# Kernel optimization log

Hardware: AMD Instinct MI355X
Metric: run time of the kernel (lower is better)

The kernel has to match this reference:

```python
import jax, jax.numpy as jnp
import numpy as np

N_NODES = 100_000
N_EDGES = 1_000_000
H = 128
NUM_STATES = 4
UPPER_T, LOWER_T, NUM_ITERS, TEMP_EVAL = 1.0, 0.1, 10000, 0.1


def temp_by_step(step, upper, lower, num_iters, temp_eval):
    # Python-level schedule: eval temp at step == -1, else linear anneal.
    if step == -1:
        return temp_eval
    frac = min(step / num_iters, 1.0)
    return upper + (lower - upper) * frac


def from_binary_states(states):
    # [*, k] bits -> integer id in [0, 2**k)
    weights = 2 ** jnp.arange(states.shape[-1])
    return (states * weights).sum(-1)


def setup_inputs() -> dict:
    key = jax.random.key(0)
    ks = jax.random.split(key, 20)
    N, E, h = N_NODES, N_EDGES, H
    node_states = jax.random.randint(ks[0], (N, NUM_STATES), 0, 2)
    edge_states = jax.random.randint(ks[1], (E, NUM_STATES), 0, 2)
    scalars = jax.random.normal(ks[2], (E, 1), jnp.float32)
    # first N edges are self-loops ordered by node id (required by the module's
    # node_scalars = scalars[src == dst] indexing convention)
    loops = jnp.arange(N)
    src = jax.random.randint(ks[3], (E - N,), 0, N)
    dst = jax.random.randint(ks[4], (E - N,), 0, N)
    dst = jnp.where(dst == src, (dst + 1) % N, dst)  # no accidental self-loops
    edge_index = jnp.stack([jnp.concatenate([loops, src]),
                            jnp.concatenate([loops, dst])])
    batched_reverse_idx = jax.random.randint(ks[5], (E,), 0, E)
    batch_scalars = jax.random.normal(ks[6], (E, 1, 1), jnp.float32)
    s = 0.02
    params = dict(
        node_emb=s * jax.random.normal(ks[7], (2 ** NUM_STATES, h), jnp.float32),
        edge_emb=s * jax.random.normal(ks[8], (2 ** NUM_STATES, h), jnp.float32),
        combine_W=s * jax.random.normal(ks[9], (2 * h, h), jnp.float32),
        combine_b=jnp.zeros((h,), jnp.float32),
        keep_W=s * jax.random.normal(ks[10], (h, 2), jnp.float32),
        keep_b=jnp.zeros((2,), jnp.float32),
        push_W=s * jax.random.normal(ks[11], (h, 2), jnp.float32),
        push_b=jnp.zeros((2,), jnp.float32),
        push_node_W=s * jax.random.normal(ks[12], (h, 2), jnp.float32),
        push_node_b=jnp.zeros((2,), jnp.float32),
        increment_W=s * jax.random.normal(ks[13], (h, 2), jnp.float32),
        increment_b=jnp.zeros((2,), jnp.float32),
    )
    return dict(node_states=node_states, edge_states=edge_states, scalars=scalars,
                edge_index=edge_index, batched_reverse_idx=batched_reverse_idx,
                batch_scalars=batch_scalars, processor_step=0, training_step=0,
                **params)


def reference(node_states, edge_states, scalars, edge_index, batched_reverse_idx,
              batch_scalars, processor_step, training_step,
              node_emb, edge_emb, combine_W, combine_b, keep_W, keep_b,
              push_W, push_b, push_node_W, push_node_b,
              increment_W, increment_b):
    N = node_states.shape[0]
    tau = temp_by_step(int(training_step), UPPER_T, LOWER_T, NUM_ITERS, TEMP_EVAL)
    # use_noise = config.use_noise (False) and training_step != -1 -> False

    node_fts = node_emb[from_binary_states(node_states)]   # [N, h]
    edge_fts = edge_emb[from_binary_states(edge_states)]   # [E, h]
    src, dst = edge_index[0], edge_index[1]
    fts = jnp.concatenate([edge_fts[batched_reverse_idx], node_fts[src]], axis=1)
    fts = fts @ combine_W + combine_b                       # [E, h]

    s = scalars.reshape(-1)                                 # [E]

    def pair_gumbel_first(W, b):
        # grouped (per-edge pair) softmax; take first component (== [::2])
        logits = (fts @ W + b) / tau                        # [E, 2]
        return jax.nn.softmax(logits, axis=-1)[:, 0]

    increment = 1.0 * pair_gumbel_first(increment_W, increment_b)
    keep = s * pair_gumbel_first(keep_W, keep_b)

    # push: first N edges are self-loops, self-loop of node i is edge i
    push_wo = pair_gumbel_first(push_W, push_b)
    push_w = pair_gumbel_first(push_node_W, push_node_b)
    node_scalars = s[:N]                                    # scalars at self-loops
    s_wo = s - node_scalars[dst]
    s_w = s_wo + node_scalars[src]
    acc = (jax.ops.segment_sum(push_wo * s_wo, dst, num_segments=N)
           + jax.ops.segment_sum(push_w * s_w, dst, num_segments=N))  # [N]
    edge_push = jnp.zeros_like(s).at[:N].set(acc)           # nonzero only on self-loops

    new_scalars = (increment + keep + edge_push)[:, None]   # [E, 1]
    target = batch_scalars[:, processor_step]               # [E, 1]
    loss = jnp.mean((target - new_scalars) ** 2)
    return new_scalars, loss
```

## Files before the change

kernel.cpp:

```cpp
#include <hip/hip_runtime.h>
#include <math.h>
#include <stdint.h>

#define N_NODES 100000
#define N_EDGES 1000000
#define HDIM 128
#define N_NONLOOP (N_EDGES - N_NODES)

typedef float  vfloat4 __attribute__((ext_vector_type(4)));
typedef int    vint4   __attribute__((ext_vector_type(4)));

__device__ __forceinline__ float get_invtau(const int* __restrict__ training_step) {
    int step = training_step[0];
    float tau;
    if (step == -1) {
        tau = 0.1f;
    } else {
        float frac = fminf((float)step / 10000.0f, 1.0f);
        tau = 1.0f + (0.1f - 1.0f) * frac;
    }
    return 1.0f / tau;
}

__device__ __forceinline__ float wave_reduce(float v) {
    #pragma unroll
    for (int off = 32; off > 0; off >>= 1) v += __shfl_down(v, off, 64);
    return v;
}

#define TAB_BLOCKS  33
#define NODE_BLOCKS 391
#define EI_BLOCKS   977

__global__ __launch_bounds__(256) void fused_pre(
    const int* __restrict__ node_states,
    const float* __restrict__ s,
    const int* __restrict__ edge_states,
    const float* __restrict__ node_emb,
    const float* __restrict__ edge_emb,
    const float* __restrict__ cW, const float* __restrict__ cb,
    const float* __restrict__ kW, const float* __restrict__ kb,
    const float* __restrict__ pW, const float* __restrict__ pb,
    const float* __restrict__ pnW, const float* __restrict__ pnb,
    const float* __restrict__ iW, const float* __restrict__ ib,
    const int* __restrict__ tstep,
    float2* __restrict__ node_pack,
    float* __restrict__ acc,
    uint8_t* __restrict__ ei,
    float* __restrict__ tabs,
    float* __restrict__ loss_out)
{
    const int b = blockIdx.x;

    if (b < TAB_BLOCKS) {
        const int w    = b * 4 + (threadIdx.x >> 6);
        const int lane = threadIdx.x & 63;
        if (w >= 132) return;
        const float invtau = get_invtau(tstep);

        if (w < 128) {
            const int isB = w >> 6, h = (w >> 4) & 3, i = w & 15;
            const float* emb = isB ? node_emb : edge_emb;
            const float* cWh = cW + isB * 128 * 128;
            float t0 = 0.f, t1 = 0.f;
            #pragma unroll 4
            for (int l = 0; l < 128; ++l) {
                const float el = emb[i * 128 + l];
                t0 += el * cWh[l * 128 + lane];
                t1 += el * cWh[l * 128 + 64 + lane];
            }
            const float* W = (h == 0) ? kW : (h == 1) ? pW : (h == 2) ? pnW : iW;
            const float wd0 = W[2 * lane] - W[2 * lane + 1];
            const float wd1 = W[2 * (lane + 64)] - W[2 * (lane + 64) + 1];
            float p = t0 * wd0 + t1 * wd1;
            p = wave_reduce(p);
            if (lane == 0) tabs[isB * 64 + i * 4 + h] = p * invtau;
        } else {
            const int h = w & 3;
            const float* W = (h == 0) ? kW : (h == 1) ? pW : (h == 2) ? pnW : iW;
            const float wd0 = W[2 * lane] - W[2 * lane + 1];
            const float wd1 = W[2 * (lane + 64)] - W[2 * (lane + 64) + 1];
            float p = cb[lane] * wd0 + cb[64 + lane] * wd1;
            p = wave_reduce(p);
            if (lane == 0) {
                const float* bb = (h == 0) ? kb : (h == 1) ? pb : (h == 2) ? pnb : ib;
                tabs[128 + h] = (p + bb[0] - bb[1]) * invtau;
            }
        }
        return;
    }

    if (b < TAB_BLOCKS + NODE_BLOCKS) {
        const int n = (b - TAB_BLOCKS) * 256 + threadIdx.x;
        if (n == 0) *loss_out = 0.f;
        if (n < N_NODES) {
            vint4 st = __builtin_nontemporal_load(&((const vint4*)node_states)[n]);
            const int idx = st.x + 2 * st.y + 4 * st.z + 8 * st.w;
            float2 np;
            np.x = s[n];
            np.y = __int_as_float(idx);
            node_pack[n] = np;
            acc[n] = 0.f;
        }
        return;
    }

    const int t = (b - TAB_BLOCKS - NODE_BLOCKS) * 256 + threadIdx.x;
    if (t < N_EDGES / 4) {
        const vint4* esp = (const vint4*)edge_states + 4 * t;
        vint4 e0 = __builtin_nontemporal_load(esp + 0);
        vint4 e1 = __builtin_nontemporal_load(esp + 1);
        vint4 e2 = __builtin_nontemporal_load(esp + 2);
        vint4 e3 = __builtin_nontemporal_load(esp + 3);
        const uint32_t i0 = e0.x + 2 * e0.y + 4 * e0.z + 8 * e0.w;
        const uint32_t i1 = e1.x + 2 * e1.y + 4 * e1.z + 8 * e1.w;
        const uint32_t i2 = e2.x + 2 * e2.y + 4 * e2.z + 8 * e2.w;
        const uint32_t i3 = e3.x + 2 * e3.y + 4 * e3.z + 8 * e3.w;
        ((uint32_t*)ei)[t] = i0 | (i1 << 8) | (i2 << 16) | (i3 << 24);
    }
}

__global__ __launch_bounds__(256) void edge_kernel(
    const float* __restrict__ s,
    const int* __restrict__ src,
    const int* __restrict__ dst,
    const int* __restrict__ brev,
    const uint8_t* __restrict__ ei,
    const float2* __restrict__ node_pack,
    const float* __restrict__ tabs,
    const float* __restrict__ target,
    float* __restrict__ acc,
    float* __restrict__ out,
    float* __restrict__ loss_out)
{
    __shared__ float4 sf[33];
    if (threadIdx.x < 33) sf[threadIdx.x] = ((const float4*)tabs)[threadIdx.x];
    __syncthreads();

    const int t = blockIdx.x * blockDim.x + threadIdx.x;
    const bool active = (t < N_NONLOOP / 4);
    float lsum = 0.f;
    float ov[4], av[4];
    int   dsv[4];
    int   g = 0;

    if (active) {
        g = (N_NODES / 4) + t;
        const vint4   rv = __builtin_nontemporal_load(&((const vint4*)brev)[g]);
        const vint4   sr = __builtin_nontemporal_load(&((const vint4*)src)[g]);
        const vint4   ds = __builtin_nontemporal_load(&((const vint4*)dst)[g]);
        const vfloat4 sv = __builtin_nontemporal_load(&((const vfloat4*)s)[g]);
        const vfloat4 tg = __builtin_nontemporal_load(&((const vfloat4*)target)[g]);

        const int rvv[4] = {rv.x, rv.y, rv.z, rv.w};
        const int srv[4] = {sr.x, sr.y, sr.z, sr.w};
        dsv[0] = ds.x; dsv[1] = ds.y; dsv[2] = ds.z; dsv[3] = ds.w;
        const float svv[4] = {sv.x, sv.y, sv.z, sv.w};
        const float tgv[4] = {tg.x, tg.y, tg.z, tg.w};

        int    eidx[4];
        float2 np[4];
        float  sd[4];
        #pragma unroll
        for (int j = 0; j < 4; ++j) {
            eidx[j] = ei[rvv[j]];
            np[j]   = node_pack[srv[j]];
            sd[j]   = node_pack[dsv[j]].x;
        }

        const float4 c4 = sf[32];
        #pragma unroll
        for (int j = 0; j < 4; ++j) {
            const int   ni = __float_as_int(np[j].y);
            const float ss = np[j].x;
            const float4 a = sf[eidx[j]];
            const float4 b = sf[16 + ni];
            const float lk  = a.x + b.x + c4.x;
            const float lp  = a.y + b.y + c4.y;
            const float lpn = a.z + b.z + c4.z;
            const float li  = a.w + b.w + c4.w;
            const float pk  = 1.f / (1.f + __expf(-lk));
            const float pp  = 1.f / (1.f + __expf(-lp));
            const float ppn = 1.f / (1.f + __expf(-lpn));
            const float pi  = 1.f / (1.f + __expf(-li));

            const float s_wo = svv[j] - sd[j];
            const float s_w  = s_wo + ss;
            av[j] = pp * s_wo + ppn * s_w;

            ov[j] = pi + svv[j] * pk;
            const float d = tgv[j] - ov[j];
            lsum += d * d;
        }
    }

    lsum = wave_reduce(lsum);
    __shared__ float wsum[4];
    const int lane = threadIdx.x & 63, wid = threadIdx.x >> 6;
    if (lane == 0) wsum[wid] = lsum;
    __syncthreads();
    if (threadIdx.x == 0) {
        const float tot = wsum[0] + wsum[1] + wsum[2] + wsum[3];
        atomicAdd(loss_out, tot * (1.0f / (float)N_EDGES));
    }

    if (active) {
        #pragma unroll
        for (int j = 0; j < 4; ++j)
            unsafeAtomicAdd(&acc[dsv[j]], av[j]);
        vfloat4 o4 = {ov[0], ov[1], ov[2], ov[3]};
        __builtin_nontemporal_store(o4, &((vfloat4*)out)[g]);
    }
}

__global__ __launch_bounds__(256) void finalize_nodes(
    const int* __restrict__ brev,
    const uint8_t* __restrict__ ei,
    const float2* __restrict__ node_pack,
    const float* __restrict__ tabs,
    const float* __restrict__ target,
    const float* __restrict__ acc,
    float* __restrict__ out,
    float* __restrict__ loss_out)
{
    __shared__ float4 sf[33];
    if (threadIdx.x < 33) sf[threadIdx.x] = ((const float4*)tabs)[threadIdx.x];
    __syncthreads();

    const int n = blockIdx.x * blockDim.x + threadIdx.x;
    const bool active = (n < N_NODES);
    float sq = 0.f, v = 0.f;
    if (active) {
        const int    rev = brev[n];
        const int    eidx = ei[rev];
        const float2 np  = node_pack[n];
        const int    ni  = __float_as_int(np.y);
        const float  sv  = np.x;

        const float4 a  = sf[eidx];
        const float4 b  = sf[16 + ni];
        const float4 c4 = sf[32];
        const float lk  = a.x + b.x + c4.x;
        const float lpn = a.z + b.z + c4.z;
        const float li  = a.w + b.w + c4.w;
        const float pk  = 1.f / (1.f + __expf(-lk));
        const float ppn = 1.f / (1.f + __expf(-lpn));
        const float pi  = 1.f / (1.f + __expf(-li));

        v = pi + sv * (pk + ppn) + acc[n];
        const float d = target[n] - v;
        sq = d * d;
    }
    sq = wave_reduce(sq);
    __shared__ float wsum[4];
    const int lane = threadIdx.x & 63, wid = threadIdx.x >> 6;
    if (lane == 0) wsum[wid] = sq;
    __syncthreads();
    if (threadIdx.x == 0) {
        const float tot = wsum[0] + wsum[1] + wsum[2] + wsum[3];
        atomicAdd(loss_out, tot * (1.0f / (float)N_EDGES));
    }
    if (active) out[n] = v;
}

extern "C" void kernel_launch(void* const* d_in, const int* in_sizes, int n_in,
                              void* d_out, int out_size, void* d_ws, size_t ws_size,
                              hipStream_t stream) {
    const int*   node_states   = (const int*)d_in[0];
    const int*   edge_states   = (const int*)d_in[1];
    const float* scalars       = (const float*)d_in[2];
    const int*   edge_index    = (const int*)d_in[3];
    const int*   brev          = (const int*)d_in[4];
    const float* batch_scalars = (const float*)d_in[5];
    const int*   training_step = (const int*)d_in[7];
    const float* node_emb  = (const float*)d_in[8];
    const float* edge_emb  = (const float*)d_in[9];
    const float* combine_W = (const float*)d_in[10];
    const float* combine_b = (const float*)d_in[11];
    const float* keep_W  = (const float*)d_in[12];
    const float* keep_b  = (const float*)d_in[13];
    const float* push_W  = (const float*)d_in[14];
    const float* push_b  = (const float*)d_in[15];
    const float* pushn_W = (const float*)d_in[16];
    const float* pushn_b = (const float*)d_in[17];
    const float* inc_W   = (const float*)d_in[18];
    const float* inc_b   = (const float*)d_in[19];

    float* out = (float*)d_out;

    char* ws = (char*)d_ws;
    float*   tabs      = (float*)ws;
    float*   acc       = (float*)(ws + 1024);
    float2*  node_pack = (float2*)(ws + 1024 + (size_t)N_NODES * 4);
    uint8_t* ei        = (uint8_t*)(ws + 1024 + (size_t)N_NODES * 12);

    const int* srcp = edge_index;
    const int* dstp = edge_index + N_EDGES;

    fused_pre<<<TAB_BLOCKS + NODE_BLOCKS + EI_BLOCKS, 256, 0, stream>>>(
        node_states, scalars, edge_states, node_emb, edge_emb,
        combine_W, combine_b, keep_W, keep_b, push_W, push_b,
        pushn_W, pushn_b, inc_W, inc_b, training_step,
        node_pack, acc, ei, tabs, out + N_EDGES);

    const int ethreads = N_NONLOOP / 4;
    edge_kernel<<<(ethreads + 255) / 256, 256, 0, stream>>>(
        scalars, srcp, dstp, brev, ei, node_pack, tabs, batch_scalars,
        acc, out, out + N_EDGES);

    finalize_nodes<<<(N_NODES + 255) / 256, 256, 0, stream>>>(
        brev, ei, node_pack, tabs, batch_scalars, acc, out, out + N_EDGES);
}
```

Before: 187.4 us.

## Privatize node accumulators per XCD and use non-coherent L2-scoped atomics

The edge kernel reads the hardware XCC id and scatters its push contributions into a per-XCD copy of the node accumulator, using a raw global_atomic_add_f32 with no system scope. The aim is to keep atomics inside each die's L2 rather than resolving them device-wide. finalize_nodes then sums the 8 copies, and the loss partials are handled the same way. Separately, the table precompute is split across 132 blocks with 4 waves each, and the per-node edge-state index is computed up front, so finalize no longer does a dependent brev->ei gather. Risks: correctness depends on the L2 atomics being visible to the next kernel on another XCD, and there is extra memory traffic to zero and read the 8 accumulator copies.

```diff
diff --git a/kernel.cpp b/kernel.cpp
--- a/kernel.cpp
+++ b/kernel.cpp
@@ -4,11 +4,21 @@
 
 #define N_NODES 100000
 #define N_EDGES 1000000
-#define HDIM 128
 #define N_NONLOOP (N_EDGES - N_NODES)
+#define NXCD 8
 
 typedef float  vfloat4 __attribute__((ext_vector_type(4)));
 typedef int    vint4   __attribute__((ext_vector_type(4)));
+
+#define XCC_ID_HWREG (20 | ((4 - 1) << 11))
+
+__device__ __forceinline__ int get_xcc() {
+    return __builtin_amdgcn_s_getreg(XCC_ID_HWREG) & (NXCD - 1);
+}
+
+__device__ __forceinline__ void l2_atomic_add(float* p, float v) {
+    asm volatile("global_atomic_add_f32 %0, %1, off" :: "v"(p), "v"(v) : "memory");
+}
 
 __device__ __forceinline__ float get_invtau(const int* __restrict__ training_step) {
     int step = training_step[0];
@@ -28,7 +38,7 @@
     return v;
 }
 
-#define TAB_BLOCKS  33
+#define TAB_BLOCKS  132
 #define NODE_BLOCKS 391
 #define EI_BLOCKS   977
 
@@ -36,6 +46,7 @@
     const int* __restrict__ node_states,
     const float* __restrict__ s,
     const int* __restrict__ edge_states,
+    const int* __restrict__ brev,
     const float* __restrict__ node_emb,
     const float* __restrict__ edge_emb,
     const float* __restrict__ cW, const float* __restrict__ cb,
@@ -47,24 +58,30 @@
     float2* __restrict__ node_pack,
     float* __restrict__ acc,
     uint8_t* __restrict__ ei,
+    uint8_t* __restrict__ eib_node,
     float* __restrict__ tabs,
-    float* __restrict__ loss_out)
+    float* __restrict__ lossp,
+    float* __restrict__ loss_out,
+    int ncopies)
 {
     const int b = blockIdx.x;
 
     if (b < TAB_BLOCKS) {
-        const int w    = b * 4 + (threadIdx.x >> 6);
+        const int w    = b;
         const int lane = threadIdx.x & 63;
-        if (w >= 132) return;
+        const int wv   = threadIdx.x >> 6;
         const float invtau = get_invtau(tstep);
-
+        __shared__ float part[4];
+
+        float p = 0.f;
         if (w < 128) {
             const int isB = w >> 6, h = (w >> 4) & 3, i = w & 15;
             const float* emb = isB ? node_emb : edge_emb;
             const float* cWh = cW + isB * 128 * 128;
             float t0 = 0.f, t1 = 0.f;
-            #pragma unroll 4
-            for (int l = 0; l < 128; ++l) {
+            const int l0 = wv * 32;
+            #pragma unroll 8
+            for (int l = l0; l < l0 + 32; ++l) {
                 const float el = emb[i * 128 + l];
                 t0 += el * cWh[l * 128 + lane];
                 t1 += el * cWh[l * 128 + 64 + lane];
@@ -72,19 +89,26 @@
             const float* W = (h == 0) ? kW : (h == 1) ? pW : (h == 2) ? pnW : iW;
             const float wd0 = W[2 * lane] - W[2 * lane + 1];
             const float wd1 = W[2 * (lane + 64)] - W[2 * (lane + 64) + 1];
-            float p = t0 * wd0 + t1 * wd1;
-            p = wave_reduce(p);
-            if (lane == 0) tabs[isB * 64 + i * 4 + h] = p * invtau;
-        } else {
+            p = t0 * wd0 + t1 * wd1;
+        } else if (wv == 0) {
             const int h = w & 3;
             const float* W = (h == 0) ? kW : (h == 1) ? pW : (h == 2) ? pnW : iW;
             const float wd0 = W[2 * lane] - W[2 * lane + 1];
             const float wd1 = W[2 * (lane + 64)] - W[2 * (lane + 64) + 1];
-            float p = cb[lane] * wd0 + cb[64 + lane] * wd1;
-            p = wave_reduce(p);
-            if (lane == 0) {
+            p = cb[lane] * wd0 + cb[64 + lane] * wd1;
+        }
+        p = wave_reduce(p);
+        if (lane == 0) part[wv] = p;
+        __syncthreads();
+        if (threadIdx.x == 0) {
+            const float tot = part[0] + part[1] + part[2] + part[3];
+            if (w < 128) {
+                const int isB = w >> 6, h = (w >> 4) & 3, i = w & 15;
+                tabs[isB * 64 + i * 4 + h] = tot * invtau;
+            } else {
+                const int h = w & 3;
                 const float* bb = (h == 0) ? kb : (h == 1) ? pb : (h == 2) ? pnb : ib;
-                tabs[128 + h] = (p + bb[0] - bb[1]) * invtau;
+                tabs[128 + h] = (tot + bb[0] - bb[1]) * invtau;
             }
         }
         return;
@@ -92,6 +116,7 @@
 
     if (b < TAB_BLOCKS + NODE_BLOCKS) {
         const int n = (b - TAB_BLOCKS) * 256 + threadIdx.x;
+        if (n < 256) lossp[n] = 0.f;
         if (n == 0) *loss_out = 0.f;
         if (n < N_NODES) {
             vint4 st = __builtin_nontemporal_load(&((const vint4*)node_states)[n]);
@@ -100,7 +125,10 @@
             np.x = s[n];
             np.y = __int_as_float(idx);
             node_pack[n] = np;
-            acc[n] = 0.f;
+            for (int k = 0; k < ncopies; ++k) acc[(size_t)k * N_NODES + n] = 0.f;
+            const int rev = brev[n];
+            const int4 est = ((const int4*)edge_states)[rev];
+            eib_node[n] = (uint8_t)(est.x + 2 * est.y + 4 * est.z + 8 * est.w);
         }
         return;
     }
@@ -120,6 +148,7 @@
     }
 }
 
+template<int MODE>
 __global__ __launch_bounds__(256) void edge_kernel(
     const float* __restrict__ s,
     const int* __restrict__ src,
@@ -130,12 +159,20 @@
     const float* __restrict__ tabs,
     const float* __restrict__ target,
     float* __restrict__ acc,
+    float* __restrict__ lossp,
     float* __restrict__ out,
     float* __restrict__ loss_out)
 {
     __shared__ float4 sf[33];
     if (threadIdx.x < 33) sf[threadIdx.x] = ((const float4*)tabs)[threadIdx.x];
     __syncthreads();
+
+    int xcc = 0;
+    float* accx = acc;
+    if (MODE == 1) {
+        xcc  = get_xcc();
+        accx = acc + (size_t)xcc * N_NODES;
+    }
 
     const int t = blockIdx.x * blockDim.x + threadIdx.x;
     const bool active = (t < N_NONLOOP / 4);
@@ -200,26 +237,30 @@
     if (lane == 0) wsum[wid] = lsum;
     __syncthreads();
     if (threadIdx.x == 0) {
-        const float tot = wsum[0] + wsum[1] + wsum[2] + wsum[3];
-        atomicAdd(loss_out, tot * (1.0f / (float)N_EDGES));
+        const float tot = (wsum[0] + wsum[1] + wsum[2] + wsum[3]) * (1.0f / (float)N_EDGES);
+        if (MODE == 1) l2_atomic_add(&lossp[xcc * 32], tot);
+        else           atomicAdd(loss_out, tot);
     }
 
     if (active) {
         #pragma unroll
-        for (int j = 0; j < 4; ++j)
-            unsafeAtomicAdd(&acc[dsv[j]], av[j]);
+        for (int j = 0; j < 4; ++j) {
+            if (MODE == 1) l2_atomic_add(&accx[dsv[j]], av[j]);
+            else           unsafeAtomicAdd(&acc[dsv[j]], av[j]);
+        }
         vfloat4 o4 = {ov[0], ov[1], ov[2], ov[3]};
         __builtin_nontemporal_store(o4, &((vfloat4*)out)[g]);
     }
 }
 
+template<int NC>
 __global__ __launch_bounds__(256) void finalize_nodes(
-    const int* __restrict__ brev,
-    const uint8_t* __restrict__ ei,
+    const uint8_t* __restrict__ eib_node,
     const float2* __restrict__ node_pack,
     const float* __restrict__ tabs,
     const float* __restrict__ target,
     const float* __restrict__ acc,
+    const float* __restrict__ lossp,
     float* __restrict__ out,
     float* __restrict__ loss_out)
 {
@@ -231,11 +272,14 @@
     const bool active = (n < N_NODES);
     float sq = 0.f, v = 0.f;
     if (active) {
-        const int    rev = brev[n];
-        const int    eidx = ei[rev];
+        const int    eidx = eib_node[n];
         const float2 np  = node_pack[n];
         const int    ni  = __float_as_int(np.y);
         const float  sv  = np.x;
+
+        float a8 = 0.f;
+        #pragma unroll
+        for (int k = 0; k < NC; ++k) a8 += acc[(size_t)k * N_NODES + n];
 
         const float4 a  = sf[eidx];
         const float4 b  = sf[16 + ni];
@@ -247,7 +291,7 @@
         const float ppn = 1.f / (1.f + __expf(-lpn));
         const float pi  = 1.f / (1.f + __expf(-li));
 
-        v = pi + sv * (pk + ppn) + acc[n];
+        v = pi + sv * (pk + ppn) + a8;
         const float d = target[n] - v;
         sq = d * d;
     }
@@ -257,8 +301,12 @@
     if (lane == 0) wsum[wid] = sq;
     __syncthreads();
     if (threadIdx.x == 0) {
-        const float tot = wsum[0] + wsum[1] + wsum[2] + wsum[3];
-        atomicAdd(loss_out, tot * (1.0f / (float)N_EDGES));
+        float tot = (wsum[0] + wsum[1] + wsum[2] + wsum[3]) * (1.0f / (float)N_EDGES);
+        if (blockIdx.x == 0) {
+            #pragma unroll
+            for (int k = 0; k < NXCD; ++k) tot += lossp[k * 32];
+        }
+        atomicAdd(loss_out, tot);
     }
     if (active) out[n] = v;
 }
@@ -288,26 +336,41 @@
 
     float* out = (float*)d_out;
 
+    const size_t need_scoped = 2048 + (size_t)NXCD * N_NODES * 4 + (size_t)N_NODES * 8
+                             + N_EDGES + N_NODES + 1024;
+    const bool scoped = (ws_size >= need_scoped);
+    const int nc = scoped ? NXCD : 1;
+
     char* ws = (char*)d_ws;
     float*   tabs      = (float*)ws;
-    float*   acc       = (float*)(ws + 1024);
-    float2*  node_pack = (float2*)(ws + 1024 + (size_t)N_NODES * 4);
-    uint8_t* ei        = (uint8_t*)(ws + 1024 + (size_t)N_NODES * 12);
+    float*   lossp     = (float*)(ws + 1024);
+    float*   acc       = (float*)(ws + 2048);
+    float2*  node_pack = (float2*)(ws + 2048 + (size_t)nc * N_NODES * 4);
+    uint8_t* ei        = (uint8_t*)node_pack + (size_t)N_NODES * 8;
+    uint8_t* eib_node  = ei + N_EDGES;
 
     const int* srcp = edge_index;
     const int* dstp = edge_index + N_EDGES;
 
     fused_pre<<<TAB_BLOCKS + NODE_BLOCKS + EI_BLOCKS, 256, 0, stream>>>(
-        node_states, scalars, edge_states, node_emb, edge_emb,
+        node_states, scalars, edge_states, brev, node_emb, edge_emb,
         combine_W, combine_b, keep_W, keep_b, push_W, push_b,
         pushn_W, pushn_b, inc_W, inc_b, training_step,
-        node_pack, acc, ei, tabs, out + N_EDGES);
+        node_pack, acc, ei, eib_node, tabs, lossp, out + N_EDGES, nc);
 
     const int ethreads = N_NONLOOP / 4;
-    edge_kernel<<<(ethreads + 255) / 256, 256, 0, stream>>>(
-        scalars, srcp, dstp, brev, ei, node_pack, tabs, batch_scalars,
-        acc, out, out + N_EDGES);
-
-    finalize_nodes<<<(N_NODES + 255) / 256, 256, 0, stream>>>(
-        brev, ei, node_pack, tabs, batch_scalars, acc, out, out + N_EDGES);
-}
+    const int eblocks  = (ethreads + 255) / 256;
+    if (scoped) {
+        edge_kernel<1><<<eblocks, 256, 0, stream>>>(
+            scalars, srcp, dstp, brev, ei, node_pack, tabs, batch_scalars,
+            acc, lossp, out, out + N_EDGES);
+        finalize_nodes<NXCD><<<(N_NODES + 255) / 256, 256, 0, stream>>>(
+            eib_node, node_pack, tabs, batch_scalars, acc, lossp, out, out + N_EDGES);
+    } else {
+        edge_kernel<0><<<eblocks, 256, 0, stream>>>(
+            scalars, srcp, dstp, brev, ei, node_pack, tabs, batch_scalars,
+            acc, lossp, out, out + N_EDGES);
+        finalize_nodes<1><<<(N_NODES + 255) / 256, 256, 0, stream>>>(
+            eib_node, node_pack, tabs, batch_scalars, acc, lossp, out, out + N_EDGES);
+    }
+}
```

Measured after the change: 180.0 us. 4.0% less time.
